# Kernel tuning notes

Measured on AMD Instinct MI355X. Metric: run time of the kernel, lower is better.

Reference implementation:

```python
import jax, jax.numpy as jnp
import numpy as np

D, H, DH, DF = 128, 8, 16, 512
N_Q, N_KV, E = 20000, 20000, 640000


def _xavier(key, shape):
    fan_in, fan_out = shape[1], shape[0]
    lim = float(np.sqrt(6.0 / (fan_in + fan_out)))
    return jax.random.uniform(key, shape, jnp.float32, -lim, lim)


def layer_norm(x, g, b, eps=1e-5):
    mu = jnp.mean(x, axis=-1, keepdims=True)
    var = jnp.var(x, axis=-1, keepdims=True)
    return (x - mu) * jax.lax.rsqrt(var + eps) * g + b


def setup_inputs() -> dict:
    key = jax.random.key(0)
    ks = jax.random.split(key, 12)
    return {
        "q_feat": jax.random.normal(ks[0], (N_Q, D), jnp.float32),
        "kv_feat": jax.random.normal(ks[1], (N_KV, D), jnp.float32),
        "src": jax.random.randint(ks[2], (E,), 0, N_KV, jnp.int32),
        "dst": jax.random.randint(ks[3], (E,), 0, N_Q, jnp.int32),
        "Wq": _xavier(ks[4], (H * DH, D)),
        "Wk": _xavier(ks[5], (H * DH, D)),
        "Wv": _xavier(ks[6], (H * DH, D)),
        "Wo": _xavier(ks[7], (D, H * DH)),
        "W1": _xavier(ks[8], (DF, D)),
        "bf1": jnp.zeros((DF,), jnp.float32),
        "W2": _xavier(ks[9], (D, DF)),
        "bf2": jnp.zeros((D,), jnp.float32),
        "ln1_g": jnp.ones((D,), jnp.float32),
        "ln1_b": jnp.zeros((D,), jnp.float32),
        "ln2_g": jnp.ones((D,), jnp.float32),
        "ln2_b": jnp.zeros((D,), jnp.float32),
    }


def reference(q_feat, kv_feat, src, dst, Wq, Wk, Wv, Wo, W1, bf1, W2, bf2,
              ln1_g, ln1_b, ln2_g, ln2_b):
    n_q = q_feat.shape[0]
    # projections -> [N, H, DH]
    q = (q_feat @ Wq.T).reshape(-1, H, DH)
    k = (kv_feat @ Wk.T).reshape(-1, H, DH)
    v = (kv_feat @ Wv.T).reshape(-1, H, DH)
    # edge scores: u_mul_v then sum over d_head, scaled (score per edge per head)
    score = jnp.einsum('ehd,ehd->eh', k[src], q[dst]) / np.sqrt(DH)
    # edge_softmax grouped by destination node
    mx = jax.ops.segment_max(score, dst, num_segments=n_q)  # [Nq, H]
    ex = jnp.exp(score - mx[dst])
    denom = jax.ops.segment_sum(ex, dst, num_segments=n_q)
    att = ex / denom[dst]  # [E, H]
    # weighted scatter-sum of values to destination nodes
    msg = v[src] * att[:, :, None]  # [E, H, DH]
    out = jax.ops.segment_sum(msg, dst, num_segments=n_q)  # [Nq, H, DH]
    sa = out.reshape(n_q, H * DH) @ Wo.T
    feat = layer_norm(q_feat + sa, ln1_g, ln1_b)
    ff = jax.nn.relu(feat @ W1.T + bf1) @ W2.T + bf2
    return layer_norm(feat + ff, ln2_g, ln2_b)
```

## Files before the change

kernel.cpp:

```cpp
#include <hip/hip_runtime.h>
#include <hip/hip_fp16.h>
#include <math.h>
#include <type_traits>

#define D 128
#define NH 8
#define DHD 16
#define DF 512
#define NSH 8
#define SSL 64

typedef _Float16 half8 __attribute__((ext_vector_type(8)));
typedef _Float16 half4 __attribute__((ext_vector_type(4)));
typedef float f32x4 __attribute__((ext_vector_type(4)));

__global__ __launch_bounds__(256) void conv_kernel(
    const float* __restrict__ Wo, const float* __restrict__ W1,
    const float* __restrict__ W2,
    __half* __restrict__ wo16, __half* __restrict__ w116, __half* __restrict__ w216) {
    int g = blockIdx.x * 256 + threadIdx.x;
    if (g >= 36864) return;
    const float* s;
    __half* d;
    int idx = g;
    if (idx < 4096) { s = Wo; d = wo16; }
    else if (idx < 20480) { idx -= 4096; s = W1; d = w116; }
    else { idx -= 20480; s = W2; d = w216; }
    float4 f = ((const float4*)s)[idx];
    ushort4 o;
    o.x = __half_as_ushort(__float2half(f.x));
    o.y = __half_as_ushort(__float2half(f.y));
    o.z = __half_as_ushort(__float2half(f.z));
    o.w = __half_as_ushort(__float2half(f.w));
    ((ushort4*)d)[idx] = o;
}

__global__ __launch_bounds__(256) void fill_kernel(
    const int* __restrict__ dst, const int* __restrict__ src,
    int* __restrict__ cnt, unsigned short* __restrict__ srcg, int E) {
    int i4 = blockIdx.x * 256 + threadIdx.x;
    int sh = blockIdx.x & (NSH - 1);
    int base = i4 << 2;
    if (base >= E) return;
    if (base + 3 < E) {
        int4 d4 = ((const int4*)dst)[i4];
        int4 s4 = ((const int4*)src)[i4];
        int dd[4] = {d4.x, d4.y, d4.z, d4.w};
        int ss[4] = {s4.x, s4.y, s4.z, s4.w};
#pragma unroll
        for (int u = 0; u < 4; ++u) {
            int p = atomicAdd(&cnt[dd[u] * NSH + sh], 1);
            if (p < SSL)
                srcg[((size_t)dd[u] << 9) + (sh << 6) + p] = (unsigned short)ss[u];
        }
    } else {
        for (int u = 0; u < 4 && base + u < E; ++u) {
            int dn = dst[base + u];
            int sn = src[base + u];
            int p = atomicAdd(&cnt[dn * NSH + sh], 1);
            if (p < SSL)
                srcg[((size_t)dn << 9) + (sh << 6) + p] = (unsigned short)sn;
        }
    }
}

__global__ __launch_bounds__(256) void proj_kernel(
    const float* __restrict__ q_feat, const float* __restrict__ kv_feat,
    const float* __restrict__ Wq, const float* __restrict__ Wk,
    const float* __restrict__ Wv,
    __half* __restrict__ fq, __half* __restrict__ fkv, int NQ, int NKV) {
    __shared__ __align__(16) __half As[64 * 128];
    __shared__ __align__(16) __half Ws[64 * 128];

    int xt = blockIdx.x;
    int tid = threadIdx.x;

    const float* A = xt ? kv_feat : q_feat;
    __half* C = xt ? fkv : fq;
    int O = xt ? 256 : 128;
    int NCT = xt ? 4 : 2;
    int N = xt ? NKV : NQ;
    int row0 = blockIdx.y * 64;
    if (row0 >= N) return;

    int lane = tid & 63;
    int w = tid >> 6;
    int l16 = lane & 15, lq = lane >> 4;

#pragma unroll
    for (int i = 0; i < 4; ++i) {
        int f = tid + i * 256;
        int ln = f & 63;
        int mt = (f >> 6) & 3;
        int kc = f >> 8;
        int m = row0 + mt * 16 + (ln & 15);
        int k = kc * 32 + (ln >> 4) * 8;
        half8 v = {};
        if (m < N) {
            const float4* p = (const float4*)(A + (size_t)m * 128 + k);
            float4 f0 = p[0], f1 = p[1];
            v = (half8){(_Float16)f0.x, (_Float16)f0.y, (_Float16)f0.z, (_Float16)f0.w,
                        (_Float16)f1.x, (_Float16)f1.y, (_Float16)f1.z, (_Float16)f1.w};
        }
        ((half8*)As)[f] = v;
    }

    for (int ct = 0; ct < NCT; ++ct) {
        __syncthreads();
#pragma unroll
        for (int i = 0; i < 4; ++i) {
            int f = tid + i * 256;
            int ln = f & 63;
            int nt = (f >> 6) & 3;
            int kc = f >> 8;
            int n = ct * 64 + nt * 16 + (ln & 15);
            int k = kc * 32 + (ln >> 4) * 8;
            const float* Wsrc;
            int r;
            if (xt == 0) {
                Wsrc = Wq; r = n;
            } else {
                int h = n >> 5, qd = (n >> 3) & 3, isv = (n >> 2) & 1, d2 = n & 3;
                r = h * 16 + qd * 4 + d2;
                Wsrc = isv ? Wv : Wk;
            }
            const float4* p = (const float4*)(Wsrc + (size_t)r * 128 + k);
            float4 f0 = p[0], f1 = p[1];
            ((half8*)Ws)[f] = (half8){(_Float16)f0.x, (_Float16)f0.y, (_Float16)f0.z, (_Float16)f0.w,
                                      (_Float16)f1.x, (_Float16)f1.y, (_Float16)f1.z, (_Float16)f1.w};
        }
        __syncthreads();
        f32x4 acc[4];
#pragma unroll
        for (int j = 0; j < 4; ++j) acc[j] = (f32x4){0.f, 0.f, 0.f, 0.f};
#pragma unroll
        for (int kc = 0; kc < 4; ++kc) {
            half8 a = ((half8*)As)[(kc * 4 + w) * 64 + lane];
            half8 b[4];
#pragma unroll
            for (int j = 0; j < 4; ++j) b[j] = ((half8*)Ws)[(kc * 4 + j) * 64 + lane];
#pragma unroll
            for (int j = 0; j < 4; ++j)
                acc[j] = __builtin_amdgcn_mfma_f32_16x16x32_f16(a, b[j], acc[j], 0, 0, 0);
        }
#pragma unroll
        for (int j = 0; j < 4; ++j) {
            int c = ct * 64 + j * 16 + l16;
#pragma unroll
            for (int r = 0; r < 4; ++r) {
                int row = row0 + w * 16 + lq * 4 + r;
                if (row < N) C[(size_t)row * O + c] = __float2half(acc[j][r]);
            }
        }
    }
}


__global__ __launch_bounds__(256) void attn_kernel(
    const __half* __restrict__ q, const __half* __restrict__ kv,
    const unsigned short* __restrict__ srcg, const int* __restrict__ cnt,
    __half* __restrict__ out, int NQ) {
    __shared__ unsigned short list[4][NSH * SSL];
    int wv = threadIdx.x >> 6;
    int n = blockIdx.x * 4 + wv;
    if (n >= NQ) return;
    int lane = threadIdx.x & 63;
    int eh = lane >> 5;
    int sub = lane & 31;
    int doff = sub << 2;

    const int4* c4 = (const int4*)(cnt + n * NSH);
    int4 ca = c4[0], cb = c4[1];
    int cs[8] = {ca.x, ca.y, ca.z, ca.w, cb.x, cb.y, cb.z, cb.w};
    int t0 = 0;
#pragma unroll
    for (int r = 0; r < NSH; ++r) {
        int cr = cs[r] < SSL ? cs[r] : SSL;
        if (lane < cr)
            list[wv][t0 + lane] = srcg[((size_t)n << 9) + (r << 6) + lane];
        t0 += cr;
    }
    int total = t0;

    half4 q4 = *(const half4*)(q + (size_t)n * D + doff);
    float q0 = (float)q4[0] * 0.25f, q1 = (float)q4[1] * 0.25f;
    float q2 = (float)q4[2] * 0.25f, q3 = (float)q4[3] * 0.25f;
    float lA = 0.f, lB = 0.f, lC = 0.f, lD = 0.f;
    f32x4 aA = {0.f, 0.f, 0.f, 0.f}, aB = {0.f, 0.f, 0.f, 0.f};
    f32x4 aC = {0.f, 0.f, 0.f, 0.f}, aD = {0.f, 0.f, 0.f, 0.f};
    int j = 0;
    for (; j + 8 <= total; j += 8) {
        int e0 = list[wv][j + eh];
        int e1 = list[wv][j + 2 + eh];
        int e2 = list[wv][j + 4 + eh];
        int e3 = list[wv][j + 6 + eh];
        half8 c0 = *(const half8*)(kv + (size_t)e0 * 256 + (sub << 3));
        half8 c1 = *(const half8*)(kv + (size_t)e1 * 256 + (sub << 3));
        half8 c2 = *(const half8*)(kv + (size_t)e2 * 256 + (sub << 3));
        half8 c3 = *(const half8*)(kv + (size_t)e3 * 256 + (sub << 3));
        float p0 = q0 * (float)c0[0] + q1 * (float)c0[1] + q2 * (float)c0[2] + q3 * (float)c0[3];
        float p1 = q0 * (float)c1[0] + q1 * (float)c1[1] + q2 * (float)c1[2] + q3 * (float)c1[3];
        float p2 = q0 * (float)c2[0] + q1 * (float)c2[1] + q2 * (float)c2[2] + q3 * (float)c2[3];
        float p3 = q0 * (float)c3[0] + q1 * (float)c3[1] + q2 * (float)c3[2] + q3 * (float)c3[3];
        p0 += __shfl_xor(p0, 1, 4); p0 += __shfl_xor(p0, 2, 4);
        p1 += __shfl_xor(p1, 1, 4); p1 += __shfl_xor(p1, 2, 4);
        p2 += __shfl_xor(p2, 1, 4); p2 += __shfl_xor(p2, 2, 4);
        p3 += __shfl_xor(p3, 1, 4); p3 += __shfl_xor(p3, 2, 4);
        float x0 = __expf(fminf(p0, 70.f));
        float x1 = __expf(fminf(p1, 70.f));
        float x2 = __expf(fminf(p2, 70.f));
        float x3 = __expf(fminf(p3, 70.f));
        lA += x0; lB += x1; lC += x2; lD += x3;
        aA[0] += x0 * (float)c0[4]; aA[1] += x0 * (float)c0[5];
        aA[2] += x0 * (float)c0[6]; aA[3] += x0 * (float)c0[7];
        aB[0] += x1 * (float)c1[4]; aB[1] += x1 * (float)c1[5];
        aB[2] += x1 * (float)c1[6]; aB[3] += x1 * (float)c1[7];
        aC[0] += x2 * (float)c2[4]; aC[1] += x2 * (float)c2[5];
        aC[2] += x2 * (float)c2[6]; aC[3] += x2 * (float)c2[7];
        aD[0] += x3 * (float)c3[4]; aD[1] += x3 * (float)c3[5];
        aD[2] += x3 * (float)c3[6]; aD[3] += x3 * (float)c3[7];
    }
    for (; j + 4 <= total; j += 4) {
        int e0 = list[wv][j + eh];
        int e1 = list[wv][j + 2 + eh];
        half8 c0 = *(const half8*)(kv + (size_t)e0 * 256 + (sub << 3));
        half8 c1 = *(const half8*)(kv + (size_t)e1 * 256 + (sub << 3));
        float p0 = q0 * (float)c0[0] + q1 * (float)c0[1] + q2 * (float)c0[2] + q3 * (float)c0[3];
        float p1 = q0 * (float)c1[0] + q1 * (float)c1[1] + q2 * (float)c1[2] + q3 * (float)c1[3];
        p0 += __shfl_xor(p0, 1, 4); p0 += __shfl_xor(p0, 2, 4);
        p1 += __shfl_xor(p1, 1, 4); p1 += __shfl_xor(p1, 2, 4);
        float x0 = __expf(fminf(p0, 70.f));
        float x1 = __expf(fminf(p1, 70.f));
        lA += x0; lB += x1;
        aA[0] += x0 * (float)c0[4]; aA[1] += x0 * (float)c0[5];
        aA[2] += x0 * (float)c0[6]; aA[3] += x0 * (float)c0[7];
        aB[0] += x1 * (float)c1[4]; aB[1] += x1 * (float)c1[5];
        aB[2] += x1 * (float)c1[6]; aB[3] += x1 * (float)c1[7];
    }
    for (; j < total; j += 2) {
        bool valid = (j + eh) < total;
        int e0 = list[wv][valid ? (j + eh) : 0];
        half8 c0 = *(const half8*)(kv + (size_t)e0 * 256 + (sub << 3));
        float p0 = q0 * (float)c0[0] + q1 * (float)c0[1] + q2 * (float)c0[2] + q3 * (float)c0[3];
        p0 += __shfl_xor(p0, 1, 4); p0 += __shfl_xor(p0, 2, 4);
        float x0 = valid ? __expf(fminf(p0, 70.f)) : 0.f;
        lA += x0;
        aA[0] += x0 * (float)c0[4]; aA[1] += x0 * (float)c0[5];
        aA[2] += x0 * (float)c0[6]; aA[3] += x0 * (float)c0[7];
    }
    float l = (lA + lB) + (lC + lD);
    f32x4 a;
#pragma unroll
    for (int i = 0; i < 4; ++i) a[i] = (aA[i] + aB[i]) + (aC[i] + aD[i]);
    l += __shfl_xor(l, 32);
#pragma unroll
    for (int i = 0; i < 4; ++i) a[i] += __shfl_xor(a[i], 32);
    if (eh == 0) {
        float rl = (l > 0.f) ? 1.f / l : 0.f;
        half4 o = {(_Float16)(a[0] * rl), (_Float16)(a[1] * rl),
                   (_Float16)(a[2] * rl), (_Float16)(a[3] * rl)};
        *(half4*)(out + (size_t)n * D + doff) = o;
    }
}


__device__ __forceinline__ int feat_idx64(int rr, int mt, int c) {
    return (((c >> 5) * 4 + mt) * 64 + ((c >> 3) & 3) * 16 + rr) * 8 + (c & 7);
}

__global__ __launch_bounds__(256) void tail_kernel(
    const __half* __restrict__ A , const __half* __restrict__ Wo16,
    const float* __restrict__ res1 ,
    const float* __restrict__ g1, const float* __restrict__ b1,
    const __half* __restrict__ W1h, const float* __restrict__ fb1,
    const __half* __restrict__ W2h, const float* __restrict__ fb2,
    const float* __restrict__ g2, const float* __restrict__ b2,
    float* __restrict__ out, int N) {
    __shared__ __align__(16) __half Feat[64 * 128];
    __shared__ __align__(16) __half S1[64 * 128];
    __shared__ __align__(16) __half S2[128 * 64];
    __shared__ __align__(16) __half Hs[64 * 64];
    int tid = threadIdx.x, lane = tid & 63, w = tid >> 6;
    int row0 = blockIdx.x * 64;
    int l16 = lane & 15, lq = lane >> 4;

#pragma unroll
    for (int i = 0; i < 4; ++i) {
        int f = tid + i * 256;
        int ln = f & 63, mt = (f >> 6) & 3, kc = f >> 8;
        int m = row0 + mt * 16 + (ln & 15);
        int k = kc * 32 + (ln >> 4) * 8;
        half8 av = {};
        if (m < N) av = *(const half8*)(A + (size_t)m * D + k);
        ((half8*)S1)[f] = av;
    }

    f32x4 acc[8];
#pragma unroll
    for (int j = 0; j < 8; ++j) acc[j] = (f32x4){0.f, 0.f, 0.f, 0.f};
#pragma unroll
    for (int kt = 0; kt < 2; ++kt) {
        __syncthreads();
#pragma unroll
        for (int i = 0; i < 4; ++i) {
            int f = tid + i * 256;
            int ln = f & 63, ot = (f >> 6) & 7, kc2 = f >> 9;
            int o = ot * 16 + (ln & 15);
            int k = kt * 64 + kc2 * 32 + (ln >> 4) * 8;
            ((half8*)S2)[f] = *(const half8*)(Wo16 + (size_t)o * D + k);
        }
        __syncthreads();
#pragma unroll
        for (int kc2 = 0; kc2 < 2; ++kc2) {
            half8 a = ((half8*)S1)[((kt * 2 + kc2) * 4 + w) * 64 + lane];
            half8 bf[8];
#pragma unroll
            for (int j = 0; j < 8; ++j) bf[j] = ((half8*)S2)[(kc2 * 8 + j) * 64 + lane];
#pragma unroll
            for (int j = 0; j < 8; ++j)
                acc[j] = __builtin_amdgcn_mfma_f32_16x16x32_f16(a, bf[j], acc[j], 0, 0, 0);
        }
    }
    __syncthreads();

#pragma unroll
    for (int r = 0; r < 4; ++r) {
        int rr = lq * 4 + r;
        int row = row0 + w * 16 + rr;
        bool valid = row < N;
        float vals[8];
        float s = 0.f, sq = 0.f;
#pragma unroll
        for (int j = 0; j < 8; ++j) {
            int c = j * 16 + l16;
            float v = acc[j][r];
            if (valid) v += res1[(size_t)row * D + c];
            vals[j] = v;
            s += v;
            sq += v * v;
        }
#pragma unroll
        for (int m = 1; m < 16; m <<= 1) {
            s += __shfl_xor(s, m, 16);
            sq += __shfl_xor(sq, m, 16);
        }
        float mu = s * (1.f / 128.f);
        float var = sq * (1.f / 128.f) - mu * mu;
        float inv = rsqrtf(var + 1e-5f);
#pragma unroll
        for (int j = 0; j < 8; ++j) {
            int c = j * 16 + l16;
            float o = (vals[j] - mu) * inv * g1[c] + b1[c];
            Feat[feat_idx64(rr, w, c)] = __float2half(o);
        }
    }
    __syncthreads();

    half8 a_all[4];
#pragma unroll
    for (int kc = 0; kc < 4; ++kc)
        a_all[kc] = ((half8*)Feat)[(kc * 4 + w) * 64 + lane];

    f32x4 oacc[8];
#pragma unroll
    for (int j = 0; j < 8; ++j) oacc[j] = (f32x4){0.f, 0.f, 0.f, 0.f};

    for (int hc = 0; hc < 8; ++hc) {
        __syncthreads();
#pragma unroll
        for (int i = 0; i < 4; ++i) {
            int f = tid + i * 256;
            int ln = f & 63, nt = (f >> 6) & 3, kc = f >> 8;
            int n = hc * 64 + nt * 16 + (ln & 15);
            int k = kc * 32 + (ln >> 4) * 8;
            ((half8*)S1)[f] = *(const half8*)(W1h + (size_t)n * D + k);
        }
#pragma unroll
        for (int i = 0; i < 4; ++i) {
            int f = tid + i * 256;
            int ln = f & 63, ot = (f >> 6) & 7, kc2 = f >> 9;
            int o = ot * 16 + (ln & 15);
            int k = hc * 64 + kc2 * 32 + (ln >> 4) * 8;
            ((half8*)S2)[f] = *(const half8*)(W2h + (size_t)o * DF + k);
        }
        __syncthreads();
        f32x4 hacc[4];
#pragma unroll
        for (int j = 0; j < 4; ++j) hacc[j] = (f32x4){0.f, 0.f, 0.f, 0.f};
#pragma unroll
        for (int kc = 0; kc < 4; ++kc) {
            half8 b[4];
#pragma unroll
            for (int j = 0; j < 4; ++j) b[j] = ((half8*)S1)[(kc * 4 + j) * 64 + lane];
#pragma unroll
            for (int j = 0; j < 4; ++j)
                hacc[j] = __builtin_amdgcn_mfma_f32_16x16x32_f16(a_all[kc], b[j], hacc[j], 0, 0, 0);
        }
#pragma unroll
        for (int j = 0; j < 4; ++j) {
            float bias1 = fb1[hc * 64 + j * 16 + l16];
#pragma unroll
            for (int r = 0; r < 4; ++r) {
                float v = fmaxf(hacc[j][r] + bias1, 0.f);
                int kc2 = j >> 1;
                int lanep = ((j & 1) * 2 + (l16 >> 3)) * 16 + lq * 4 + r;
                Hs[((kc2 * 4 + w) * 64 + lanep) * 8 + (l16 & 7)] = __float2half(v);
            }
        }
        __syncthreads();
#pragma unroll
        for (int kc2 = 0; kc2 < 2; ++kc2) {
            half8 a = ((half8*)Hs)[(kc2 * 4 + w) * 64 + lane];
            half8 b[8];
#pragma unroll
            for (int ot = 0; ot < 8; ++ot) b[ot] = ((half8*)S2)[(kc2 * 8 + ot) * 64 + lane];
#pragma unroll
            for (int ot = 0; ot < 8; ++ot)
                oacc[ot] = __builtin_amdgcn_mfma_f32_16x16x32_f16(a, b[ot], oacc[ot], 0, 0, 0);
        }
    }

#pragma unroll
    for (int r = 0; r < 4; ++r) {
        int rr = lq * 4 + r;
        int row = row0 + w * 16 + rr;
        bool valid = row < N;
        float vals[8];
        float s = 0.f, sq = 0.f;
#pragma unroll
        for (int j = 0; j < 8; ++j) {
            int c = j * 16 + l16;
            float v = oacc[j][r] + fb2[c] + __half2float(Feat[feat_idx64(rr, w, c)]);
            vals[j] = v;
            s += v;
            sq += v * v;
        }
#pragma unroll
        for (int m = 1; m < 16; m <<= 1) {
            s += __shfl_xor(s, m, 16);
            sq += __shfl_xor(sq, m, 16);
        }
        float mu = s * (1.f / 128.f);
        float var = sq * (1.f / 128.f) - mu * mu;
        float inv = rsqrtf(var + 1e-5f);
        if (valid) {
#pragma unroll
            for (int j = 0; j < 8; ++j) {
                int c = j * 16 + l16;
                out[(size_t)row * D + c] = (vals[j] - mu) * inv * g2[c] + b2[c];
            }
        }
    }
}


extern "C" void kernel_launch(void* const* d_in, const int* in_sizes, int n_in,
                              void* d_out, int out_size, void* d_ws, size_t ws_size,
                              hipStream_t stream) {
    const float* q_feat = (const float*)d_in[0];
    const float* kv_feat = (const float*)d_in[1];
    const int* src = (const int*)d_in[2];
    const int* dst = (const int*)d_in[3];
    const float* Wq = (const float*)d_in[4];
    const float* Wk = (const float*)d_in[5];
    const float* Wv = (const float*)d_in[6];
    const float* Wo = (const float*)d_in[7];
    const float* W1 = (const float*)d_in[8];
    const float* bf1 = (const float*)d_in[9];
    const float* W2 = (const float*)d_in[10];
    const float* bf2 = (const float*)d_in[11];
    const float* ln1g = (const float*)d_in[12];
    const float* ln1b = (const float*)d_in[13];
    const float* ln2g = (const float*)d_in[14];
    const float* ln2b = (const float*)d_in[15];

    int NQ = in_sizes[0] / D;
    int NKV = in_sizes[1] / D;
    int E = in_sizes[2];
    float* out = (float*)d_out;

    char* base = (char*)d_ws;
    size_t off = 0;
    auto alloc = [&](size_t bytes) -> void* {
        void* p = base + off;
        off += (bytes + 255) & ~(size_t)255;
        return p;
    };
    __half* fq16 = (__half*)alloc((size_t)NQ * D * 2);
    __half* fkv = (__half*)alloc((size_t)NKV * 256 * 2);
    __half* fattn16 = (__half*)alloc((size_t)NQ * D * 2);
    int* cnt = (int*)alloc((size_t)NQ * NSH * 4);
    unsigned short* srcg = (unsigned short*)alloc((size_t)NQ * NSH * SSL * 2);
    __half* wo16 = (__half*)alloc((size_t)D * D * 2);
    __half* w116 = (__half*)alloc((size_t)DF * D * 2);
    __half* w216 = (__half*)alloc((size_t)D * DF * 2);

    hipMemsetAsync(cnt, 0, (size_t)NQ * NSH * sizeof(int), stream);

    dim3 blk(256);
    conv_kernel<<<(36864 + 255) / 256, blk, 0, stream>>>(Wo, W1, W2, wo16, w116, w216);

    int fillBlocks = (E + 1023) / 1024;
    fill_kernel<<<fillBlocks, blk, 0, stream>>>(dst, src, cnt, srcg, E);

    int NMX = NQ > NKV ? NQ : NKV;
    int ytiles = (NMX + 63) / 64;
    proj_kernel<<<dim3(2, ytiles), blk, 0, stream>>>(
        q_feat, kv_feat, Wq, Wk, Wv, fq16, fkv, NQ, NKV);

    attn_kernel<<<(NQ + 3) / 4, blk, 0, stream>>>(fq16, fkv, srcg, cnt, fattn16, NQ);

    tail_kernel<<<(NQ + 63) / 64, blk, 0, stream>>>(
        fattn16, wo16, q_feat, ln1g, ln1b, w116, bf1, w216, bf2, ln2g, ln2b, out, NQ);
}
```

Baseline: 228.0 us.

## Prefetch FFN weights into registers and merge tail kernel shared buffers

Restructures the tail kernel. Wo is loaded in one shot before a single barrier, and the W1/W2 chunks are double-buffered through registers so global loads for the next chunk overlap the current chunk's MFMA work. The residual is preloaded into registers. The Feat and Hs LDS buffers are merged into one buffer, with the LN1 result kept in registers for the final residual, and launch bounds request 3 blocks per CU. This is meant to hide global load latency and raise occupancy, at the cost of more register pressure that could cause spills.

```diff
diff --git a/kernel.cpp b/kernel.cpp
--- a/kernel.cpp
+++ b/kernel.cpp
@@ -268,7 +268,7 @@
     return (((c >> 5) * 4 + mt) * 64 + ((c >> 3) & 3) * 16 + rr) * 8 + (c & 7);
 }
 
-__global__ __launch_bounds__(256) void tail_kernel(
+__global__ __launch_bounds__(256, 3) void tail_kernel(
     const __half* __restrict__ A , const __half* __restrict__ Wo16,
     const float* __restrict__ res1 ,
     const float* __restrict__ g1, const float* __restrict__ b1,
@@ -276,14 +276,14 @@
     const __half* __restrict__ W2h, const float* __restrict__ fb2,
     const float* __restrict__ g2, const float* __restrict__ b2,
     float* __restrict__ out, int N) {
-    __shared__ __align__(16) __half Feat[64 * 128];
     __shared__ __align__(16) __half S1[64 * 128];
     __shared__ __align__(16) __half S2[128 * 64];
-    __shared__ __align__(16) __half Hs[64 * 64];
+    __shared__ __align__(16) __half FH[64 * 128];
     int tid = threadIdx.x, lane = tid & 63, w = tid >> 6;
     int row0 = blockIdx.x * 64;
     int l16 = lane & 15, lq = lane >> 4;
 
+    half8 rA[4], rW[8];
 #pragma unroll
     for (int i = 0; i < 4; ++i) {
         int f = tid + i * 256;
@@ -292,36 +292,155 @@
         int k = kc * 32 + (ln >> 4) * 8;
         half8 av = {};
         if (m < N) av = *(const half8*)(A + (size_t)m * D + k);
-        ((half8*)S1)[f] = av;
-    }
-
-    f32x4 acc[8];
-#pragma unroll
-    for (int j = 0; j < 8; ++j) acc[j] = (f32x4){0.f, 0.f, 0.f, 0.f};
-#pragma unroll
-    for (int kt = 0; kt < 2; ++kt) {
-        __syncthreads();
+        rA[i] = av;
+    }
+#pragma unroll
+    for (int i = 0; i < 8; ++i) {
+        int f = tid + (i & 3) * 256;
+        int kt = i >> 2;
+        int ln = f & 63, ot = (f >> 6) & 7, kc2 = f >> 9;
+        int o = ot * 16 + (ln & 15);
+        int k = kt * 64 + kc2 * 32 + (ln >> 4) * 8;
+        rW[i] = *(const half8*)(Wo16 + (size_t)o * D + k);
+    }
+#pragma unroll
+    for (int i = 0; i < 4; ++i) ((half8*)FH)[tid + i * 256] = rA[i];
+#pragma unroll
+    for (int i = 0; i < 4; ++i) ((half8*)S1)[tid + i * 256] = rW[i];
+#pragma unroll
+    for (int i = 0; i < 4; ++i) ((half8*)S2)[tid + i * 256] = rW[4 + i];
+    __syncthreads();
+
+    half8 r1[4], r2[4];
+    auto ldw = [&](int hcx) {
+#pragma unroll
+        for (int i = 0; i < 4; ++i) {
+            int f = tid + i * 256;
+            int ln = f & 63, nt = (f >> 6) & 3, kc = f >> 8;
+            int n = hcx * 64 + nt * 16 + (ln & 15);
+            int k = kc * 32 + (ln >> 4) * 8;
+            r1[i] = *(const half8*)(W1h + (size_t)n * D + k);
+        }
 #pragma unroll
         for (int i = 0; i < 4; ++i) {
             int f = tid + i * 256;
             int ln = f & 63, ot = (f >> 6) & 7, kc2 = f >> 9;
             int o = ot * 16 + (ln & 15);
-            int k = kt * 64 + kc2 * 32 + (ln >> 4) * 8;
-            ((half8*)S2)[f] = *(const half8*)(Wo16 + (size_t)o * D + k);
-        }
+            int k = hcx * 64 + kc2 * 32 + (ln >> 4) * 8;
+            r2[i] = *(const half8*)(W2h + (size_t)o * DF + k);
+        }
+    };
+    ldw(0);
+    float rres[4][8];
+#pragma unroll
+    for (int r = 0; r < 4; ++r) {
+        int row = row0 + w * 16 + lq * 4 + r;
+        bool valid = row < N;
+#pragma unroll
+        for (int j = 0; j < 8; ++j)
+            rres[r][j] = valid ? res1[(size_t)row * D + j * 16 + l16] : 0.f;
+    }
+
+    f32x4 acc[8];
+#pragma unroll
+    for (int j = 0; j < 8; ++j) acc[j] = (f32x4){0.f, 0.f, 0.f, 0.f};
+#pragma unroll
+    for (int kc = 0; kc < 4; ++kc) {
+        half8 a = ((half8*)FH)[(kc * 4 + w) * 64 + lane];
+        const __half* Sx = (kc < 2) ? S1 : S2;
+        int kc2 = kc & 1;
+        half8 bf[8];
+#pragma unroll
+        for (int j = 0; j < 8; ++j) bf[j] = ((half8*)Sx)[(kc2 * 8 + j) * 64 + lane];
+#pragma unroll
+        for (int j = 0; j < 8; ++j)
+            acc[j] = __builtin_amdgcn_mfma_f32_16x16x32_f16(a, bf[j], acc[j], 0, 0, 0);
+    }
+    __syncthreads();
+
+    half8 fres[4];
+#pragma unroll
+    for (int r = 0; r < 4; ++r) {
+        int rr = lq * 4 + r;
+        float vals[8];
+        float s = 0.f, sq = 0.f;
+#pragma unroll
+        for (int j = 0; j < 8; ++j) {
+            float v = acc[j][r] + rres[r][j];
+            vals[j] = v;
+            s += v;
+            sq += v * v;
+        }
+#pragma unroll
+        for (int m = 1; m < 16; m <<= 1) {
+            s += __shfl_xor(s, m, 16);
+            sq += __shfl_xor(sq, m, 16);
+        }
+        float mu = s * (1.f / 128.f);
+        float var = sq * (1.f / 128.f) - mu * mu;
+        float inv = rsqrtf(var + 1e-5f);
+#pragma unroll
+        for (int j = 0; j < 8; ++j) {
+            int c = j * 16 + l16;
+            float o = (vals[j] - mu) * inv * g1[c] + b1[c];
+            FH[feat_idx64(rr, w, c)] = __float2half(o);
+            fres[r][j] = (_Float16)o;
+        }
+    }
+    __syncthreads();
+
+    half8 a_all[4];
+#pragma unroll
+    for (int kc = 0; kc < 4; ++kc)
+        a_all[kc] = ((half8*)FH)[(kc * 4 + w) * 64 + lane];
+
+    f32x4 oacc[8];
+#pragma unroll
+    for (int j = 0; j < 8; ++j) oacc[j] = (f32x4){0.f, 0.f, 0.f, 0.f};
+
+    for (int hc = 0; hc < 8; ++hc) {
         __syncthreads();
 #pragma unroll
+        for (int i = 0; i < 4; ++i) ((half8*)S1)[tid + i * 256] = r1[i];
+#pragma unroll
+        for (int i = 0; i < 4; ++i) ((half8*)S2)[tid + i * 256] = r2[i];
+        if (hc < 7) ldw(hc + 1);
+        __syncthreads();
+        f32x4 hacc[4];
+#pragma unroll
+        for (int j = 0; j < 4; ++j) hacc[j] = (f32x4){0.f, 0.f, 0.f, 0.f};
+#pragma unroll
+        for (int kc = 0; kc < 4; ++kc) {
+            half8 b[4];
+#pragma unroll
+            for (int j = 0; j < 4; ++j) b[j] = ((half8*)S1)[(kc * 4 + j) * 64 + lane];
+#pragma unroll
+            for (int j = 0; j < 4; ++j)
+                hacc[j] = __builtin_amdgcn_mfma_f32_16x16x32_f16(a_all[kc], b[j], hacc[j], 0, 0, 0);
+        }
+#pragma unroll
+        for (int j = 0; j < 4; ++j) {
+            float bias1 = fb1[hc * 64 + j * 16 + l16];
+#pragma unroll
+            for (int r = 0; r < 4; ++r) {
+                float v = fmaxf(hacc[j][r] + bias1, 0.f);
+                int kc2 = j >> 1;
+                int lanep = ((j & 1) * 2 + (l16 >> 3)) * 16 + lq * 4 + r;
+                FH[((kc2 * 4 + w) * 64 + lanep) * 8 + (l16 & 7)] = __float2half(v);
+            }
+        }
+        __syncthreads();
+#pragma unroll
         for (int kc2 = 0; kc2 < 2; ++kc2) {
-            half8 a = ((half8*)S1)[((kt * 2 + kc2) * 4 + w) * 64 + lane];
-            half8 bf[8];
-#pragma unroll
-            for (int j = 0; j < 8; ++j) bf[j] = ((half8*)S2)[(kc2 * 8 + j) * 64 + lane];
-#pragma unroll
-            for (int j = 0; j < 8; ++j)
-                acc[j] = __builtin_amdgcn_mfma_f32_16x16x32_f16(a, bf[j], acc[j], 0, 0, 0);
-        }
-    }
-    __syncthreads();
+            half8 a = ((half8*)FH)[(kc2 * 4 + w) * 64 + lane];
+            half8 b[8];
+#pragma unroll
+            for (int ot = 0; ot < 8; ++ot) b[ot] = ((half8*)S2)[(kc2 * 8 + ot) * 64 + lane];
+#pragma unroll
+            for (int ot = 0; ot < 8; ++ot)
+                oacc[ot] = __builtin_amdgcn_mfma_f32_16x16x32_f16(a, b[ot], oacc[ot], 0, 0, 0);
+        }
+    }
 
 #pragma unroll
     for (int r = 0; r < 4; ++r) {
@@ -333,104 +452,7 @@
 #pragma unroll
         for (int j = 0; j < 8; ++j) {
             int c = j * 16 + l16;
-            float v = acc[j][r];
-            if (valid) v += res1[(size_t)row * D + c];
-            vals[j] = v;
-            s += v;
-            sq += v * v;
-        }
-#pragma unroll
-        for (int m = 1; m < 16; m <<= 1) {
-            s += __shfl_xor(s, m, 16);
-            sq += __shfl_xor(sq, m, 16);
-        }
-        float mu = s * (1.f / 128.f);
-        float var = sq * (1.f / 128.f) - mu * mu;
-        float inv = rsqrtf(var + 1e-5f);
-#pragma unroll
-        for (int j = 0; j < 8; ++j) {
-            int c = j * 16 + l16;
-            float o = (vals[j] - mu) * inv * g1[c] + b1[c];
-            Feat[feat_idx64(rr, w, c)] = __float2half(o);
-        }
-    }
-    __syncthreads();
-
-    half8 a_all[4];
-#pragma unroll
-    for (int kc = 0; kc < 4; ++kc)
-        a_all[kc] = ((half8*)Feat)[(kc * 4 + w) * 64 + lane];
-
-    f32x4 oacc[8];
-#pragma unroll
-    for (int j = 0; j < 8; ++j) oacc[j] = (f32x4){0.f, 0.f, 0.f, 0.f};
-
-    for (int hc = 0; hc < 8; ++hc) {
-        __syncthreads();
-#pragma unroll
-        for (int i = 0; i < 4; ++i) {
-            int f = tid + i * 256;
-            int ln = f & 63, nt = (f >> 6) & 3, kc = f >> 8;
-            int n = hc * 64 + nt * 16 + (ln & 15);
-            int k = kc * 32 + (ln >> 4) * 8;
-            ((half8*)S1)[f] = *(const half8*)(W1h + (size_t)n * D + k);
-        }
-#pragma unroll
-        for (int i = 0; i < 4; ++i) {
-            int f = tid + i * 256;
-            int ln = f & 63, ot = (f >> 6) & 7, kc2 = f >> 9;
-            int o = ot * 16 + (ln & 15);
-            int k = hc * 64 + kc2 * 32 + (ln >> 4) * 8;
-            ((half8*)S2)[f] = *(const half8*)(W2h + (size_t)o * DF + k);
-        }
-        __syncthreads();
-        f32x4 hacc[4];
-#pragma unroll
-        for (int j = 0; j < 4; ++j) hacc[j] = (f32x4){0.f, 0.f, 0.f, 0.f};
-#pragma unroll
-        for (int kc = 0; kc < 4; ++kc) {
-            half8 b[4];
-#pragma unroll
-            for (int j = 0; j < 4; ++j) b[j] = ((half8*)S1)[(kc * 4 + j) * 64 + lane];
-#pragma unroll
-            for (int j = 0; j < 4; ++j)
-                hacc[j] = __builtin_amdgcn_mfma_f32_16x16x32_f16(a_all[kc], b[j], hacc[j], 0, 0, 0);
-        }
-#pragma unroll
-        for (int j = 0; j < 4; ++j) {
-            float bias1 = fb1[hc * 64 + j * 16 + l16];
-#pragma unroll
-            for (int r = 0; r < 4; ++r) {
-                float v = fmaxf(hacc[j][r] + bias1, 0.f);
-                int kc2 = j >> 1;
-                int lanep = ((j & 1) * 2 + (l16 >> 3)) * 16 + lq * 4 + r;
-                Hs[((kc2 * 4 + w) * 64 + lanep) * 8 + (l16 & 7)] = __float2half(v);
-            }
-        }
-        __syncthreads();
-#pragma unroll
-        for (int kc2 = 0; kc2 < 2; ++kc2) {
-            half8 a = ((half8*)Hs)[(kc2 * 4 + w) * 64 + lane];
-            half8 b[8];
-#pragma unroll
-            for (int ot = 0; ot < 8; ++ot) b[ot] = ((half8*)S2)[(kc2 * 8 + ot) * 64 + lane];
-#pragma unroll
-            for (int ot = 0; ot < 8; ++ot)
-                oacc[ot] = __builtin_amdgcn_mfma_f32_16x16x32_f16(a, b[ot], oacc[ot], 0, 0, 0);
-        }
-    }
-
-#pragma unroll
-    for (int r = 0; r < 4; ++r) {
-        int rr = lq * 4 + r;
-        int row = row0 + w * 16 + rr;
-        bool valid = row < N;
-        float vals[8];
-        float s = 0.f, sq = 0.f;
-#pragma unroll
-        for (int j = 0; j < 8; ++j) {
-            int c = j * 16 + l16;
-            float v = oacc[j][r] + fb2[c] + __half2float(Feat[feat_idx64(rr, w, c)]);
+            float v = oacc[j][r] + fb2[c] + (float)fres[r][j];
             vals[j] = v;
             s += v;
             sq += v * v;
```

New measurement: 220.8 us. -3.2%, faster.
